# Kernel optimization log

Measured on AMD Instinct MI355X. Metric: run time of the kernel, lower is better.

The kernel has to match this reference:

```python
import jax, jax.numpy as jnp
import numpy as np

G = 64          # graphs in batch
NODES = 512     # nodes per graph
CAND = 2048     # edge candidates per graph
D = 256         # in_dim
H = 256         # hid_size
ENS = 2         # ensemble
N = G * NODES   # 32768 total nodes
E = G * CAND    # 131072 total candidate edges


def setup_inputs() -> dict:
    key = jax.random.key(0)
    ks = jax.random.split(key, 8)
    s = lambda fan: 1.0 / np.sqrt(fan)
    node_feat = jax.random.normal(ks[0], (N, D), jnp.float32)
    edge_candidate = jax.random.randint(ks[1], (E, 2), 0, NODES, jnp.int32)
    nnodes = jnp.full((G,), NODES, jnp.int32)
    num_edge_candidate = jnp.full((G,), CAND, jnp.int32)
    W_enc = jax.random.normal(ks[2], (D, D), jnp.float32) * s(D)
    b_enc = jnp.zeros((D,), jnp.float32)
    W1 = jax.random.normal(ks[3], (2 * D, H), jnp.float32) * s(2 * D)
    b1 = jnp.zeros((H,), jnp.float32)
    W2 = jax.random.normal(ks[4], (H, H), jnp.float32) * s(H)
    b2 = jnp.zeros((H,), jnp.float32)
    W3 = jax.random.normal(ks[5], (H, ENS), jnp.float32) * s(H)
    b3 = jnp.zeros((ENS,), jnp.float32)
    return {
        'node_feat': node_feat, 'edge_candidate': edge_candidate,
        'nnodes': nnodes, 'num_edge_candidate': num_edge_candidate,
        'W_enc': W_enc, 'b_enc': b_enc,
        'W1': W1, 'b1': b1, 'W2': W2, 'b2': b2, 'W3': W3, 'b3': b3,
    }


def reference(node_feat, edge_candidate, nnodes, num_edge_candidate,
              W_enc, b_enc, W1, b1, W2, b2, W3, b3):
    # atom encoder (linear stand-in): x [N, D]
    x = node_feat @ W_enc + b_enc
    # per-graph node offsets: [0, cumsum(nnodes)[:-1]]
    edge_rel = jnp.concatenate([jnp.zeros((1,), nnodes.dtype), jnp.cumsum(nnodes)[:-1]])
    offsets = jnp.repeat(edge_rel, num_edge_candidate,
                         total_repeat_length=edge_candidate.shape[0])
    edge_candidate_idx = edge_candidate + offsets[:, None]  # [E, 2] global indices
    # gather endpoint embeddings and concat: [E, 2D]
    h = jnp.concatenate([x[edge_candidate_idx[:, 0]], x[edge_candidate_idx[:, 1]]], axis=-1)
    # MLP: Linear+ReLU, Linear+ReLU, Linear
    h = jax.nn.relu(h @ W1 + b1)
    h = jax.nn.relu(h @ W2 + b2)
    scores = h @ W3 + b3  # [E, ENS]
    return scores, edge_candidate_idx
```

## Files before the change

### kernel.cpp

```cpp
#include <hip/hip_runtime.h>
#include <hip/hip_bf16.h>

typedef short short8 __attribute__((ext_vector_type(8)));
typedef float f32x4 __attribute__((ext_vector_type(4)));

__device__ __forceinline__ ushort f2bf(float f) {
    union { float f; unsigned u; } v; v.f = f;
    unsigned r = v.u + 0x7fff + ((v.u >> 16) & 1);
    return (ushort)(r >> 16);
}

__device__ __forceinline__ void gload_lds16(const void* g, void* l) {
    __builtin_amdgcn_global_load_lds((const __attribute__((address_space(1))) void*)g,
                                     (__attribute__((address_space(3))) void*)l, 16, 0, 0);
}


__global__ __launch_bounds__(256) void prep_k(
    const float* __restrict__ node_feat, ushort* __restrict__ nf_bf, int n4,
    const int* __restrict__ ec, const int* __restrict__ nnodes, const int* __restrict__ ncand,
    int G, int E, int* __restrict__ idxb, float* __restrict__ out_idx,
    const float* __restrict__ W2, ushort* __restrict__ pk2,
    const float* __restrict__ We, const float* __restrict__ be,
    const float* __restrict__ W1, const float* __restrict__ b1,
    ushort* __restrict__ pk1, float* __restrict__ bc)
{
    const int b = blockIdx.x;
    if (b < 2048) {
        int i = b * 256 + threadIdx.x;
        const int stride = 2048 * 256;
        for (int j = i; j < n4; j += stride) {
            float4 v = ((const float4*)node_feat)[j];
            ushort4 o;
            o.x = f2bf(v.x); o.y = f2bf(v.y); o.z = f2bf(v.z); o.w = f2bf(v.w);
            ((ushort4*)nf_bf)[j] = o;
        }
    } else if (b < 2560) {
        __shared__ int snoff[257];
        __shared__ int seoff[257];
        if (threadIdx.x == 0) {
            int a = 0, c = 0;
            for (int g = 0; g < G; g++) {
                snoff[g] = a; a += nnodes[g];
                c += ncand[g]; seoff[g] = c;
            }
        }
        __syncthreads();
        int e = (b - 2048) * 256 + threadIdx.x;
        if (e >= E) return;
        int lo = 0, hi = G - 1;
        while (lo < hi) {
            int mid = (lo + hi) >> 1;
            if (seoff[mid] > e) hi = mid; else lo = mid + 1;
        }
        int off = snoff[lo];
        int g0 = ec[2 * e] + off, g1 = ec[2 * e + 1] + off;
        idxb[2 * e] = g0; idxb[2 * e + 1] = g1;
        out_idx[2 * e] = (float)g0; out_idx[2 * e + 1] = (float)g1;
    } else if (b < 2816) {
        int id = (b - 2560) * 256 + threadIdx.x;
        int j = id & 7;
        int l = (id >> 3) & 63;
        int S = (id >> 9) & 7;
        int F = id >> 12;
        int n = F * 16 + (l & 15);
        int k = S * 32 + (l >> 4) * 8 + j;
        pk2[id] = f2bf(W2[(size_t)k * 256 + n]);
    } else {
        int k = b - 2816;
        int n = threadIdx.x;
        if (k < 512) {
            const float* werow = We + (size_t)(k & 255) * 256;
            const float* w1col = W1 + ((k >> 8) ? 256 * 256 : 0);
            float acc = 0.f;
#pragma unroll 4
            for (int d = 0; d < 256; d++)
                acc += werow[d] * w1col[(size_t)d * 256 + n];
            int j = k & 7;
            int S = k >> 5;
            int F = n >> 4;
            int l = ((k >> 3) & 3) * 16 + (n & 15);
            pk1[((size_t)(F * 16 + S) * 64 + l) * 8 + j] = f2bf(acc);
        } else {
            float acc = b1[n];
#pragma unroll 4
            for (int d = 0; d < 256; d++)
                acc += be[d] * (W1[(size_t)d * 256 + n] + W1[(size_t)(d + 256) * 256 + n]);
            bc[n] = acc;
        }
    }
}


#define LOADB(bk, Bp, KDIV32, t)                                                            \
    _Pragma("unroll") for (int nf = 0; nf < 2; nf++)                                        \
    _Pragma("unroll") for (int kk = 0; kk < 2; kk++)                                        \
        bk[nf * 2 + kk] = *(const short8*)&Bp[((size_t)((wn * 2 + nf) * (KDIV32)            \
                                               + (t) * 2 + kk) * 64 + l) * 8];

#define COMPUTE1(bi, bk)                                                                    \
    {                                                                                       \
        short8 af[8];                                                                       \
        _Pragma("unroll") for (int mf = 0; mf < 4; mf++)                                    \
        _Pragma("unroll") for (int kk = 0; kk < 2; kk++)                                    \
            af[mf * 2 + kk] = *(const short8*)&ring[(bi) * 8192 +                           \
                (wm * 64 + mf * 16 + llo) * 64 + (((kk * 4 + lhi) ^ (llo & 7)) * 8)];       \
        __builtin_amdgcn_s_setprio(1);                                                      \
        _Pragma("unroll") for (int mf = 0; mf < 4; mf++)                                    \
        _Pragma("unroll") for (int nf = 0; nf < 2; nf++)                                    \
        _Pragma("unroll") for (int kk = 0; kk < 2; kk++)                                    \
            acc[mf][nf] = __builtin_amdgcn_mfma_f32_16x16x32_bf16(                          \
                bk[nf * 2 + kk], af[mf * 2 + kk], acc[mf][nf], 0, 0, 0);                    \
        __builtin_amdgcn_s_setprio(0);                                                      \
    }

#define COMPUTE2(t2, bk)                                                                    \
    {                                                                                       \
        short8 af[8];                                                                       \
        _Pragma("unroll") for (int mf = 0; mf < 4; mf++)                                    \
        _Pragma("unroll") for (int kk = 0; kk < 2; kk++)                                    \
            af[mf * 2 + kk] = *(const short8*)&h1lds[                                       \
                (wm * 64 + mf * 16 + llo) * 256 +                                           \
                (((t2) * 8 | ((kk * 4 + lhi) ^ (llo & 7))) * 8)];                           \
        __builtin_amdgcn_s_setprio(1);                                                      \
        _Pragma("unroll") for (int mf = 0; mf < 4; mf++)                                    \
        _Pragma("unroll") for (int nf = 0; nf < 2; nf++)                                    \
        _Pragma("unroll") for (int kk = 0; kk < 2; kk++)                                    \
            acc[mf][nf] = __builtin_amdgcn_mfma_f32_16x16x32_bf16(                          \
                bk[nf * 2 + kk], af[mf * 2 + kk], acc[mf][nf], 0, 0, 0);                    \
        __builtin_amdgcn_s_setprio(0);                                                      \
    }

#define TILE_BARRIER(n)                                                                     \
    __builtin_amdgcn_sched_barrier(0);                                                      \
    asm volatile("s_waitcnt vmcnt(" #n ")" ::: "memory");                                   \
    __builtin_amdgcn_s_barrier();                                                           \
    __builtin_amdgcn_sched_barrier(0);

__global__ __launch_bounds__(1024, 4) void fused_mlp(
    const ushort* __restrict__ nf_bf, const int* __restrict__ idx,
    const ushort* __restrict__ pk1, const float* __restrict__ bc,
    const ushort* __restrict__ pk2, const float* __restrict__ b2,
    const float* __restrict__ W3, const float* __restrict__ b3,
    float* __restrict__ scores)
{
    __shared__ __align__(16) ushort smem[36864];
    ushort* ring = smem;
    ushort* h1lds = smem;
    float* sc = (float*)&smem[32768];

    const int tid = threadIdx.x;
    const int w = tid >> 6, l = tid & 63;
    const int llo = l & 15, lhi = l >> 4;
    const int wm = w >> 3, wn = w & 7;
    const int work = ((blockIdx.x & 7) << 7) + (blockIdx.x >> 3);
    const int m0 = work * 128;

    const int srow = tid >> 3;
    const int swz = 8 * ((l & 7) ^ ((l >> 3) & 7));
    const int2 ip = *(const int2*)&idx[2 * (m0 + srow)];
    const ushort* rp0 = nf_bf + (size_t)ip.x * 256 + swz;
    const ushort* rp1 = nf_bf + (size_t)ip.y * 256 + swz;

    f32x4 acc[4][2];
#pragma unroll
    for (int mf = 0; mf < 4; mf++)
#pragma unroll
        for (int nf = 0; nf < 2; nf++) acc[mf][nf] = {0.f, 0.f, 0.f, 0.f};

    short8 bkA[4], bkB[4];

    auto stageA = [&](int bi, int t) {
        const ushort* src = ((t < 4) ? rp0 : rp1) + ((t & 3) * 64);
        gload_lds16(src, &ring[bi * 8192 + w * 512]);
    };

    stageA(0, 0);
    LOADB(bkA, pk1, 16, 0)
    stageA(1, 1);
    stageA(2, 2);
    TILE_BARRIER(6)

#pragma unroll
    for (int t = 0; t < 8; t++) {
        if (t + 1 < 8) {
            if (t & 1) { LOADB(bkA, pk1, 16, t + 1) } else { LOADB(bkB, pk1, 16, t + 1) }
        }
        if (t + 3 < 8) stageA((t + 3) & 3, t + 3);
        if (t & 1) COMPUTE1(t & 3, bkB)
        else       COMPUTE1(t & 3, bkA)
        if (t == 0)      { TILE_BARRIER(6) }
        else if (t <= 4) { TILE_BARRIER(10) }
        else if (t == 5) { TILE_BARRIER(9) }
        else if (t == 6) { TILE_BARRIER(8) }
    }

    LOADB(bkA, pk2, 8, 0)
    __syncthreads();

    {
#pragma unroll
        for (int nf = 0; nf < 2; nf++) {
            int colb = wn * 32 + nf * 16 + lhi * 4;
            float4 bv = *(const float4*)&bc[colb];
            int c = colb >> 3;
            int coff = colb & 7;
#pragma unroll
            for (int mf = 0; mf < 4; mf++) {
                int row = wm * 64 + mf * 16 + llo;
                float v0 = fmaxf(acc[mf][nf][0] + bv.x, 0.f);
                float v1 = fmaxf(acc[mf][nf][1] + bv.y, 0.f);
                float v2 = fmaxf(acc[mf][nf][2] + bv.z, 0.f);
                float v3 = fmaxf(acc[mf][nf][3] + bv.w, 0.f);
                ushort4 o;
                o.x = f2bf(v0); o.y = f2bf(v1); o.z = f2bf(v2); o.w = f2bf(v3);
                int cs = (c & 24) | ((c & 7) ^ (row & 7));
                *(ushort4*)&h1lds[row * 256 + cs * 8 + coff] = o;
            }
        }
    }
    __syncthreads();

#pragma unroll
    for (int mf = 0; mf < 4; mf++)
#pragma unroll
        for (int nf = 0; nf < 2; nf++) acc[mf][nf] = {0.f, 0.f, 0.f, 0.f};

#pragma unroll
    for (int t2 = 0; t2 < 4; t2++) {
        if (t2 + 1 < 4) {
            if (t2 & 1) { LOADB(bkA, pk2, 8, t2 + 1) } else { LOADB(bkB, pk2, 8, t2 + 1) }
        }
        if (t2 & 1) COMPUTE2(t2, bkB)
        else        COMPUTE2(t2, bkA)
    }

    float p0[4], p1[4];
#pragma unroll
    for (int mf = 0; mf < 4; mf++) { p0[mf] = 0.f; p1[mf] = 0.f; }
#pragma unroll
    for (int nf = 0; nf < 2; nf++) {
        int colb = wn * 32 + nf * 16 + lhi * 4;
        float4 b2v = *(const float4*)&b2[colb];
        float2 w3a = ((const float2*)W3)[colb + 0];
        float2 w3b = ((const float2*)W3)[colb + 1];
        float2 w3c = ((const float2*)W3)[colb + 2];
        float2 w3d = ((const float2*)W3)[colb + 3];
#pragma unroll
        for (int mf = 0; mf < 4; mf++) {
            float v0 = fmaxf(acc[mf][nf][0] + b2v.x, 0.f);
            float v1 = fmaxf(acc[mf][nf][1] + b2v.y, 0.f);
            float v2 = fmaxf(acc[mf][nf][2] + b2v.z, 0.f);
            float v3 = fmaxf(acc[mf][nf][3] + b2v.w, 0.f);
            p0[mf] += v0 * w3a.x + v1 * w3b.x + v2 * w3c.x + v3 * w3d.x;
            p1[mf] += v0 * w3a.y + v1 * w3b.y + v2 * w3c.y + v3 * w3d.y;
        }
    }
#pragma unroll
    for (int mf = 0; mf < 4; mf++) {
        p0[mf] += __shfl_xor(p0[mf], 16); p0[mf] += __shfl_xor(p0[mf], 32);
        p1[mf] += __shfl_xor(p1[mf], 16); p1[mf] += __shfl_xor(p1[mf], 32);
    }
    if (l < 16) {
#pragma unroll
        for (int mf = 0; mf < 4; mf++) {
            int r = wm * 64 + mf * 16 + l;
            sc[(wn * 128 + r) * 2 + 0] = p0[mf];
            sc[(wn * 128 + r) * 2 + 1] = p1[mf];
        }
    }
    __syncthreads();
    if (tid < 256) {
        int row = tid >> 1, j = tid & 1;
        float s = b3[j];
#pragma unroll
        for (int q = 0; q < 8; q++) s += sc[(q * 128 + row) * 2 + j];
        scores[(size_t)(m0 + row) * 2 + j] = s;
    }
}


extern "C" void kernel_launch(void* const* d_in, const int* in_sizes, int n_in,
                              void* d_out, int out_size, void* d_ws, size_t ws_size,
                              hipStream_t stream) {
    const float* node_feat = (const float*)d_in[0];
    const int* edge_candidate = (const int*)d_in[1];
    const int* nnodes = (const int*)d_in[2];
    const int* ncand = (const int*)d_in[3];
    const float* W_enc = (const float*)d_in[4];
    const float* b_enc = (const float*)d_in[5];
    const float* W1 = (const float*)d_in[6];
    const float* b1 = (const float*)d_in[7];
    const float* W2 = (const float*)d_in[8];
    const float* b2 = (const float*)d_in[9];
    const float* W3 = (const float*)d_in[10];
    const float* b3 = (const float*)d_in[11];

    const int D = 256;
    const int G = in_sizes[2];
    const int TOTN = in_sizes[0] / D;
    const int E = in_sizes[1] / 2;
    const int ENS = in_sizes[11];

    char* wsb = (char*)d_ws;
    size_t off = 0;
    auto alloc = [&](size_t bytes) -> void* {
        void* p = wsb + off;
        off += (bytes + 255) & ~(size_t)255;
        return p;
    };
    ushort* nf_bf = (ushort*)alloc((size_t)TOTN * D * 2);
    ushort* pk1   = (ushort*)alloc((size_t)512 * 256 * 2);
    ushort* pk2   = (ushort*)alloc((size_t)256 * 256 * 2);
    float*  bc    = (float*)alloc(256 * 4);
    int* idxb     = (int*)alloc((size_t)E * 2 * 4);

    float* scores_out = (float*)d_out;
    float* idx_out = scores_out + (size_t)E * ENS;

    prep_k<<<3329, 256, 0, stream>>>(
        node_feat, nf_bf, TOTN * D / 4,
        edge_candidate, nnodes, ncand, G, E, idxb, idx_out,
        W2, pk2,
        W_enc, b_enc, W1, b1, pk1, bc);

    fused_mlp<<<E / 128, 1024, 0, stream>>>(nf_bf, idxb, pk1, bc, pk2, b2, W3, b3, scores_out);
}
```

Baseline: 81.71 us.

## Load full gathered A panel up front instead of a 4-slot ring pipeline

Replaces the 4-deep LDS ring of gathered endpoint tiles with a full 8-tile panel (128 KB LDS) loaded at kernel start. A single wait and barrier replace the per-tile vmcnt waits and barriers in the layer-1 loop. The aim is to remove intra-loop synchronization. The cost is that LDS use nearly doubles, which cuts occupancy (the launch bounds ask for 4 blocks/CU, which cannot fit), and the global-load latency is no longer overlapped with compute.

```diff
diff --git a/kernel.cpp b/kernel.cpp
--- a/kernel.cpp
+++ b/kernel.cpp
@@ -98,12 +98,12 @@
         bk[nf * 2 + kk] = *(const short8*)&Bp[((size_t)((wn * 2 + nf) * (KDIV32)            \
                                                + (t) * 2 + kk) * 64 + l) * 8];
 
-#define COMPUTE1(bi, bk)                                                                    \
+#define COMPUTE1(t, bk)                                                                     \
     {                                                                                       \
         short8 af[8];                                                                       \
         _Pragma("unroll") for (int mf = 0; mf < 4; mf++)                                    \
         _Pragma("unroll") for (int kk = 0; kk < 2; kk++)                                    \
-            af[mf * 2 + kk] = *(const short8*)&ring[(bi) * 8192 +                           \
+            af[mf * 2 + kk] = *(const short8*)&panel[(t) * 8192 +                           \
                 (wm * 64 + mf * 16 + llo) * 64 + (((kk * 4 + lhi) ^ (llo & 7)) * 8)];       \
         __builtin_amdgcn_s_setprio(1);                                                      \
         _Pragma("unroll") for (int mf = 0; mf < 4; mf++)                                    \
@@ -131,12 +131,6 @@
         __builtin_amdgcn_s_setprio(0);                                                      \
     }
 
-#define TILE_BARRIER(n)                                                                     \
-    __builtin_amdgcn_sched_barrier(0);                                                      \
-    asm volatile("s_waitcnt vmcnt(" #n ")" ::: "memory");                                   \
-    __builtin_amdgcn_s_barrier();                                                           \
-    __builtin_amdgcn_sched_barrier(0);
-
 __global__ __launch_bounds__(1024, 4) void fused_mlp(
     const ushort* __restrict__ nf_bf, const int* __restrict__ idx,
     const ushort* __restrict__ pk1, const float* __restrict__ bc,
@@ -144,10 +138,10 @@
     const float* __restrict__ W3, const float* __restrict__ b3,
     float* __restrict__ scores)
 {
-    __shared__ __align__(16) ushort smem[36864];
-    ushort* ring = smem;
+    __shared__ __align__(16) ushort smem[69632];
+    ushort* panel = smem;
     ushort* h1lds = smem;
-    float* sc = (float*)&smem[32768];
+    float* sc = (float*)&smem[65536];
 
     const int tid = threadIdx.x;
     const int w = tid >> 6, l = tid & 63;
@@ -170,53 +164,44 @@
 
     short8 bkA[4], bkB[4];
 
-    auto stageA = [&](int bi, int t) {
-        const ushort* src = ((t < 4) ? rp0 : rp1) + ((t & 3) * 64);
-        gload_lds16(src, &ring[bi * 8192 + w * 512]);
-    };
-
-    stageA(0, 0);
+#pragma unroll
+    for (int t = 0; t < 8; t++) {
+        const ushort* src = ((t < 4) ? rp0 : rp1) + ((t & 3) << 6);
+        gload_lds16(src, &panel[t * 8192 + w * 512]);
+    }
     LOADB(bkA, pk1, 16, 0)
-    stageA(1, 1);
-    stageA(2, 2);
-    TILE_BARRIER(6)
+    asm volatile("s_waitcnt vmcnt(0)" ::: "memory");
+    __builtin_amdgcn_s_barrier();
 
 #pragma unroll
     for (int t = 0; t < 8; t++) {
         if (t + 1 < 8) {
             if (t & 1) { LOADB(bkA, pk1, 16, t + 1) } else { LOADB(bkB, pk1, 16, t + 1) }
         }
-        if (t + 3 < 8) stageA((t + 3) & 3, t + 3);
-        if (t & 1) COMPUTE1(t & 3, bkB)
-        else       COMPUTE1(t & 3, bkA)
-        if (t == 0)      { TILE_BARRIER(6) }
-        else if (t <= 4) { TILE_BARRIER(10) }
-        else if (t == 5) { TILE_BARRIER(9) }
-        else if (t == 6) { TILE_BARRIER(8) }
+        if (t & 1) COMPUTE1(t, bkB)
+        else       COMPUTE1(t, bkA)
     }
 
     LOADB(bkA, pk2, 8, 0)
     __syncthreads();
 
-    {
-#pragma unroll
-        for (int nf = 0; nf < 2; nf++) {
-            int colb = wn * 32 + nf * 16 + lhi * 4;
-            float4 bv = *(const float4*)&bc[colb];
-            int c = colb >> 3;
-            int coff = colb & 7;
-#pragma unroll
-            for (int mf = 0; mf < 4; mf++) {
-                int row = wm * 64 + mf * 16 + llo;
-                float v0 = fmaxf(acc[mf][nf][0] + bv.x, 0.f);
-                float v1 = fmaxf(acc[mf][nf][1] + bv.y, 0.f);
-                float v2 = fmaxf(acc[mf][nf][2] + bv.z, 0.f);
-                float v3 = fmaxf(acc[mf][nf][3] + bv.w, 0.f);
-                ushort4 o;
-                o.x = f2bf(v0); o.y = f2bf(v1); o.z = f2bf(v2); o.w = f2bf(v3);
-                int cs = (c & 24) | ((c & 7) ^ (row & 7));
-                *(ushort4*)&h1lds[row * 256 + cs * 8 + coff] = o;
-            }
+#pragma unroll
+    for (int nf = 0; nf < 2; nf++) {
+        int colb = wn * 32 + nf * 16 + lhi * 4;
+        float4 bv = *(const float4*)&bc[colb];
+        int c = colb >> 3;
+        int coff = colb & 7;
+#pragma unroll
+        for (int mf = 0; mf < 4; mf++) {
+            int row = wm * 64 + mf * 16 + llo;
+            float v0 = fmaxf(acc[mf][nf][0] + bv.x, 0.f);
+            float v1 = fmaxf(acc[mf][nf][1] + bv.y, 0.f);
+            float v2 = fmaxf(acc[mf][nf][2] + bv.z, 0.f);
+            float v3 = fmaxf(acc[mf][nf][3] + bv.w, 0.f);
+            ushort4 o;
+            o.x = f2bf(v0); o.y = f2bf(v1); o.z = f2bf(v2); o.w = f2bf(v3);
+            int cs = (c & 24) | ((c & 7) ^ (row & 7));
+            *(ushort4*)&h1lds[row * 256 + cs * 8 + coff] = o;
         }
     }
     __syncthreads();
```

Result: slower. 83.88 us (+2.7%).
